# Kernel tuning notes

Measured on AMD Instinct MI355X. Metric: run time of the kernel, lower is better.

## Reference

```python
import jax, jax.numpy as jnp
import numpy as np

B, S, H, NH, HD = 2, 2048, 4096, 32, 128
THETA = 10000.0


def rotate_half(x):
    x1, x2 = jnp.split(x, 2, axis=-1)
    return jnp.concatenate((-x2, x1), axis=-1)


def setup_inputs() -> dict:
    key = jax.random.key(0)
    ks = jax.random.split(key, 6)
    hidden_states = jax.random.normal(ks[0], (B, S, H), dtype=jnp.float32)
    # additive causal mask, [1,1,S,S]
    causal = jnp.triu(jnp.full((S, S), -1e9, dtype=jnp.float32), k=1)
    attention_mask = causal[None, None, :, :]
    scale = 0.02
    Wq = jax.random.normal(ks[1], (H, H), dtype=jnp.float32) * scale
    Wk = jax.random.normal(ks[2], (H, H), dtype=jnp.float32) * scale
    Wv = jax.random.normal(ks[3], (H, H), dtype=jnp.float32) * scale
    Wo = jax.random.normal(ks[4], (H, H), dtype=jnp.float32) * scale
    return {"hidden_states": hidden_states, "attention_mask": attention_mask,
            "Wq": Wq, "Wk": Wk, "Wv": Wv, "Wo": Wo}


def _rope_tables(seq_len, dtype):
    inv_freq = 1.0 / (THETA ** (jnp.arange(0, HD, 2, dtype=jnp.float32) / HD))
    t = jnp.arange(seq_len, dtype=jnp.float32)
    freqs = jnp.einsum('i,j->ij', t, inv_freq)          # [S, HD/2]
    emb = jnp.concatenate((freqs, freqs), axis=-1)       # [S, HD]
    return jnp.cos(emb).astype(dtype), jnp.sin(emb).astype(dtype)


def reference(hidden_states, attention_mask, Wq, Wk, Wv, Wo):
    b, s, _ = hidden_states.shape
    # nn.Linear: y = x @ W.T
    q = jnp.einsum('bsh,oh->bso', hidden_states, Wq).reshape(b, s, NH, HD).transpose(0, 2, 1, 3)
    k = jnp.einsum('bsh,oh->bso', hidden_states, Wk).reshape(b, s, NH, HD).transpose(0, 2, 1, 3)
    v = jnp.einsum('bsh,oh->bso', hidden_states, Wv).reshape(b, s, NH, HD).transpose(0, 2, 1, 3)
    cos, sin = _rope_tables(s, q.dtype)                  # [S, HD] broadcast over b,h
    q = q * cos + rotate_half(q) * sin
    k = k * cos + rotate_half(k) * sin
    scores = jnp.einsum('bhqd,bhkd->bhqk', q, k) / jnp.sqrt(jnp.asarray(HD, q.dtype))
    scores = scores + attention_mask
    attn = jax.nn.softmax(scores.astype(jnp.float32), axis=-1).astype(q.dtype)
    out = jnp.einsum('bhqk,bhkd->bhqd', attn, v)
    out = out.transpose(0, 2, 1, 3).reshape(b, s, H)
    return jnp.einsum('bsh,oh->bso', out, Wo)
```

## Files before the change

kernel.cpp:

```cpp
#include <hip/hip_runtime.h>
#include <stdint.h>

typedef __attribute__((ext_vector_type(4))) float f32x4;
typedef __attribute__((ext_vector_type(8))) short bf16x8;
typedef __attribute__((ext_vector_type(4))) unsigned int u32x4;

__device__ __forceinline__ short f2bf(float x) {
  unsigned int u = __builtin_bit_cast(unsigned int, x);
  unsigned int r = (u + 0x7fffu + ((u >> 16) & 1u)) >> 16;
  return (short)r;
}
__device__ __forceinline__ float bf2f(short s) {
  unsigned int u = ((unsigned int)(unsigned short)s) << 16;
  return __builtin_bit_cast(float, u);
}
__device__ __forceinline__ unsigned pkbf(float lo, float hi) {
  unsigned r;
  asm("v_cvt_pk_bf16_f32 %0, %1, %2" : "=v"(r) : "v"(lo), "v"(hi));
  return r;
}

__device__ __forceinline__ void gload_lds16(const void* g, void* l) {
  __builtin_amdgcn_global_load_lds(
      (const __attribute__((address_space(1))) void*)g,
      (__attribute__((address_space(3))) void*)l, 16, 0, 0);
}

#define BARX() do { __builtin_amdgcn_s_barrier(); asm volatile("" ::: "memory"); } while (0)

__global__ __launch_bounds__(256) void cvt5(const float* __restrict__ a,
                                            const float* __restrict__ b,
                                            const float* __restrict__ c,
                                            const float* __restrict__ d,
                                            const float* __restrict__ e,
                                            short* __restrict__ oa,
                                            short* __restrict__ ob,
                                            short* __restrict__ oc,
                                            short* __restrict__ od,
                                            short* __restrict__ oe, int n) {
  int y = blockIdx.y;
  const float* in = (y == 0) ? a : (y == 1) ? b : (y == 2) ? c : (y == 3) ? d : e;
  short* out = (y == 0) ? oa : (y == 1) ? ob : (y == 2) ? oc : (y == 3) ? od : oe;
  int idx = blockIdx.x * blockDim.x + threadIdx.x;
  int stride = gridDim.x * blockDim.x;
  for (int i = idx * 4; i < n; i += stride * 4) {
    float4 v = *(const float4*)(in + i);
    short4 o;
    o.x = f2bf(v.x); o.y = f2bf(v.y); o.z = f2bf(v.z); o.w = f2bf(v.w);
    *(short4*)(out + i) = o;
  }
}

__global__ __launch_bounds__(256) void cvt_bf16(const float* __restrict__ in,
                                                short* __restrict__ out, int n) {
  int idx = blockIdx.x * blockDim.x + threadIdx.x;
  int stride = gridDim.x * blockDim.x;
  for (int i = idx * 4; i < n; i += stride * 4) {
    float4 v = *(const float4*)(in + i);
    short4 o;
    o.x = f2bf(v.x); o.y = f2bf(v.y); o.z = f2bf(v.z); o.w = f2bf(v.w);
    *(short4*)(out + i) = o;
  }
}

__global__ __launch_bounds__(256) void rope_table_k(float2* __restrict__ tab) {
  int idx = blockIdx.x * 256 + threadIdx.x;
  int s = idx >> 6, j = idx & 63;
  float invf = powf(10000.0f, -((float)j) / 64.0f);
  float a = (float)s * invf;
  tab[idx] = make_float2(cosf(a), sinf(a));
}

__global__ __launch_bounds__(256) void rope_apply_k(short* __restrict__ Qb,
                                                    short* __restrict__ Kb,
                                                    const float2* __restrict__ tab) {
  bool isK = (blockIdx.y != 0);
  short* base = isK ? Kb : Qb;
  float post = isK ? 1.0f : (0.08838834764831845f * 1.4426950408889634f);
  int token = blockIdx.x;
  int s = token & 2047;
  short* rowp = base + (size_t)token * 4096;
  const float2* trow = tab + s * 64;
  for (int u = threadIdx.x; u < 512; u += 256) {
    int h = u >> 4;
    int d0 = (u & 15) * 4;
    short* p1 = rowp + h * 128 + d0;
    short* p2 = p1 + 64;
    short4 a = *(short4*)p1, b = *(short4*)p2;
    short4 ra, rb;
#pragma unroll
    for (int j = 0; j < 4; ++j) {
      short aj = (&a.x)[j], bj = (&b.x)[j];
      float qa = bf2f(aj), qb = bf2f(bj);
      float2 cs = trow[d0 + j];
      (&ra.x)[j] = f2bf((qa * cs.x - qb * cs.y) * post);
      (&rb.x)[j] = f2bf((qb * cs.x + qa * cs.y) * post);
    }
    *(short4*)p1 = ra;
    *(short4*)p2 = rb;
  }
}

template <int MODE>
__global__ __launch_bounds__(512) void gemm8p(const short* __restrict__ A,
                                              const short* __restrict__ Bw,
                                              void* __restrict__ out) {
  __shared__ __attribute__((aligned(16))) short smem[2 * 32768];
  int wg = blockIdx.x;
  int xcd = wg & 7, ii = wg >> 3;
  int by = xcd * 2 + (ii >> 4);
  int bx = ii & 15;
  int tid = threadIdx.x;
  int w = tid >> 6, lane = tid & 63;
  int l16 = lane & 15, l4 = lane >> 4;
  int wm = w >> 2, wn = w & 3;

  f32x4 acc[8][4] = {};

  const short* Ab = A + (size_t)(by * 256) * 4096;
  const short* Bb = Bw + (size_t)(bx * 256) * 4096;

  auto STAGE_MAT = [&](int kt, int isB) {
    const short* src = isB ? Bb : Ab;
    int ob = (kt & 1) * 32768 + isB * 16384;
#pragma unroll
    for (int j = 0; j < 4; ++j) {
      int c = j * 512 + tid;
      int row = c >> 3;
      int sc = (c & 7) ^ (row & 7);
      gload_lds16(src + (size_t)row * 4096 + kt * 64 + sc * 8, &smem[ob + c * 8]);
    }
  };

  auto COMPUTE = [&](int ob) {
    bf16x8 af[4], bfr[4];
#pragma unroll
    for (int kk = 0; kk < 2; ++kk) {
#pragma unroll
      for (int nf = 0; nf < 4; ++nf) {
        int row = wn * 64 + nf * 16 + l16;
        int phys = (kk * 4 + l4) ^ (row & 7);
        bfr[nf] = *(const bf16x8*)&smem[ob + 16384 + row * 64 + phys * 8];
      }
#pragma unroll
      for (int mh = 0; mh < 2; ++mh) {
#pragma unroll
        for (int mf = 0; mf < 4; ++mf) {
          int row = wm * 128 + mh * 64 + mf * 16 + l16;
          int phys = (kk * 4 + l4) ^ (row & 7);
          af[mf] = *(const bf16x8*)&smem[ob + row * 64 + phys * 8];
        }
        __builtin_amdgcn_s_setprio(1);
#pragma unroll
        for (int mf = 0; mf < 4; ++mf)
#pragma unroll
          for (int nf = 0; nf < 4; ++nf)
            acc[mh * 4 + mf][nf] =
                __builtin_amdgcn_mfma_f32_16x16x32_bf16(af[mf], bfr[nf], acc[mh * 4 + mf][nf], 0, 0, 0);
        __builtin_amdgcn_s_setprio(0);
      }
    }
  };

  STAGE_MAT(0, 0);
  STAGE_MAT(0, 1);
  STAGE_MAT(1, 0);
  asm volatile("s_waitcnt vmcnt(4)" ::: "memory");
  BARX();

  for (int t = 0; t < 64; ++t) {
    int ob = (t & 1) * 32768;
    if (t + 1 < 64) STAGE_MAT(t + 1, 1);
    COMPUTE(ob);
    BARX();
    if (t + 2 < 64) {
      STAGE_MAT(t + 2, 0);
      asm volatile("s_waitcnt vmcnt(4)" ::: "memory");
    } else if (t + 1 < 64) {
      asm volatile("s_waitcnt vmcnt(0)" ::: "memory");
    }
    if (t + 1 < 64) BARX();
  }

  int orow0 = by * 256 + wm * 128;
  int ocol0 = bx * 256 + wn * 64;
#pragma unroll
  for (int mf = 0; mf < 8; ++mf)
#pragma unroll
    for (int nf = 0; nf < 4; ++nf)
#pragma unroll
      for (int k = 0; k < 4; ++k) {
        int r = orow0 + mf * 16 + l4 * 4 + k;
        int c = ocol0 + nf * 16 + l16;
        float v = acc[mf][nf][k];
        if constexpr (MODE == 0) {
          ((short*)out)[(size_t)r * 4096 + c] = f2bf(v);
        } else if constexpr (MODE == 1) {
          ((float*)out)[(size_t)r * 4096 + c] = v;
        } else {
          int bb = r >> 11, ss = r & 2047;
          int h = c >> 7, d = c & 127;
          ((short*)out)[(((size_t)((bb * 32 + h) * 128 + d)) << 11) + ss] = f2bf(v);
        }
      }
}

__global__ __launch_bounds__(512, 4) void attn_k(const short* __restrict__ Qb,
                                                 const short* __restrict__ Kb,
                                                 const short* __restrict__ Vt,
                                                 short* __restrict__ AO) {
  __shared__ __attribute__((aligned(16))) short smem[24576];
  int p = blockIdx.x;
  int bh = p & 63;
  int qt = 15 - (p >> 6);
  int b = bh >> 5, h = bh & 31;
  int tid = threadIdx.x, w = tid >> 6, lane = tid & 63;
  int l16 = lane & 15, l4 = lane >> 4;

  const int nt = 2 * qt + 2;
  const int qbase = qt * 128 + w * 16;

  bf16x8 qf[4];
  {
    const short* Qg = Qb + (size_t)(b * 2048 + qbase + l16) * 4096 + h * 128 + l4 * 8;
#pragma unroll
    for (int kk = 0; kk < 4; ++kk) qf[kk] = *(const bf16x8*)(Qg + kk * 32);
  }

  f32x4 oacc[8] = {};
  float mrun = -1e30f, lsum = 0.f;

  const short* Kbase = Kb + (size_t)(b * 2048) * 4096 + h * 128;
  const short* Vbase = Vt + (size_t)bh * 128 * 2048;

  auto STAGE_K = [&](int t, int sel) {
    short* lK = &smem[sel * 8192];
#pragma unroll
    for (int j = 0; j < 2; ++j) {
      int c = j * 512 + tid;
      int row = c >> 4;
      int src = (c & 15) ^ (row & 15);
      gload_lds16(Kbase + (size_t)(t * 64 + row) * 4096 + src * 8, &lK[c * 8]);
    }
  };
  auto STAGE_V = [&](int t) {
    short* lV = &smem[16384];
#pragma unroll
    for (int j = 0; j < 2; ++j) {
      int c = j * 512 + tid;
      int row = c >> 3;
      int src = (c & 7) ^ (row & 7);
      gload_lds16(Vbase + (size_t)row * 2048 + t * 64 + src * 8, &lV[c * 8]);
    }
  };

  STAGE_V(0);
  STAGE_K(0, 0);
  STAGE_K(1, 1);

  const int src0 = l16 | ((2 * (l4 & 1)) << 4);
  const int src1 = src0 | 16;
  const bool hiA = (l4 >> 1) != 0;

  for (int t = 0; t < nt; ++t) {
    if (t == nt - 1)
      asm volatile("s_waitcnt vmcnt(0)" ::: "memory");
    else
      asm volatile("s_waitcnt vmcnt(2)" ::: "memory");
    __builtin_amdgcn_s_barrier();
    asm volatile("" ::: "memory");

    bool skip = (t * 64 > qbase + 15);
    if (!skip) {
      const short* lK = &smem[(t & 1) * 8192];
      const short* lV = &smem[16384];

      f32x4 sacc[4] = {};
#pragma unroll
      for (int kk = 0; kk < 4; ++kk) {
#pragma unroll
        for (int n4 = 0; n4 < 4; ++n4) {
          int row = n4 * 16 + l16;
          int phys = (kk * 4 + l4) ^ (row & 15);
          bf16x8 kf = *(const bf16x8*)&lK[row * 128 + phys * 8];
          sacc[n4] = __builtin_amdgcn_mfma_f32_16x16x32_bf16(kf, qf[kk], sacc[n4], 0, 0, 0);
        }
      }

      if (t * 64 + 63 > qbase) {
        int q = qbase + l16;
#pragma unroll
        for (int n4 = 0; n4 < 4; ++n4)
#pragma unroll
          for (int i = 0; i < 4; ++i) {
            int kv = t * 64 + n4 * 16 + l4 * 4 + i;
            if (kv > q) sacc[n4][i] = -1e30f;
          }
      }

      {
        float v0 = fmaxf(fmaxf(sacc[0][0], sacc[0][1]), fmaxf(sacc[0][2], sacc[0][3]));
        float v1 = fmaxf(fmaxf(sacc[1][0], sacc[1][1]), fmaxf(sacc[1][2], sacc[1][3]));
        float v2 = fmaxf(fmaxf(sacc[2][0], sacc[2][1]), fmaxf(sacc[2][2], sacc[2][3]));
        float v3 = fmaxf(fmaxf(sacc[3][0], sacc[3][1]), fmaxf(sacc[3][2], sacc[3][3]));
        float vm = fmaxf(fmaxf(v0, v1), fmaxf(v2, v3));
        vm = fmaxf(vm, __shfl_xor(vm, 16));
        vm = fmaxf(vm, __shfl_xor(vm, 32));
        if (!__all(vm - mrun <= 8.0f)) {
          float mnew = fmaxf(mrun, vm);
          float fsc = __builtin_amdgcn_exp2f(mrun - mnew);
          mrun = mnew;
          lsum *= fsc;
#pragma unroll
          for (int dg = 0; dg < 8; ++dg) oacc[dg] *= fsc;
        }
        float psum = 0.f;
#pragma unroll
        for (int n4 = 0; n4 < 4; ++n4)
#pragma unroll
          for (int i = 0; i < 4; ++i) {
            float e = __builtin_amdgcn_exp2f(sacc[n4][i] - mrun);
            sacc[n4][i] = e;
            psum += e;
          }
        psum += __shfl_xor(psum, 16);
        psum += __shfl_xor(psum, 32);
        lsum += psum;
      }

#pragma unroll
      for (int c = 0; c < 2; ++c) {
        unsigned pk0h0 = pkbf(sacc[2 * c][0], sacc[2 * c][1]);
        unsigned pk0h1 = pkbf(sacc[2 * c][2], sacc[2 * c][3]);
        unsigned pk1h0 = pkbf(sacc[2 * c + 1][0], sacc[2 * c + 1][1]);
        unsigned pk1h1 = pkbf(sacc[2 * c + 1][2], sacc[2 * c + 1][3]);
        unsigned s00 = __shfl((int)pk0h0, src0), s10 = __shfl((int)pk1h0, src0);
        unsigned s01 = __shfl((int)pk0h1, src0), s11 = __shfl((int)pk1h1, src0);
        unsigned t00 = __shfl((int)pk0h0, src1), t10 = __shfl((int)pk1h0, src1);
        unsigned t01 = __shfl((int)pk0h1, src1), t11 = __shfl((int)pk1h1, src1);
        u32x4 uw;
        uw[0] = hiA ? s10 : s00;
        uw[1] = hiA ? s11 : s01;
        uw[2] = hiA ? t10 : t00;
        uw[3] = hiA ? t11 : t01;
        bf16x8 pb = __builtin_bit_cast(bf16x8, uw);
#pragma unroll
        for (int dg = 0; dg < 8; ++dg) {
          int d = dg * 16 + l16;
          int phys = (c * 4 + l4) ^ (l16 & 7);
          bf16x8 vf = *(const bf16x8*)&lV[d * 64 + phys * 8];
          oacc[dg] = __builtin_amdgcn_mfma_f32_16x16x32_bf16(vf, pb, oacc[dg], 0, 0, 0);
        }
      }
    }

    __builtin_amdgcn_s_barrier();
    asm volatile("" ::: "memory");
    if (t + 1 < nt) STAGE_V(t + 1);
    if (t + 2 < nt) STAGE_K(t + 2, t & 1);
  }

  __syncthreads();
  short* reg = &smem[w * 2048];
  float rls = 1.0f / lsum;
#pragma unroll
  for (int dg = 0; dg < 8; ++dg) {
    unsigned u0 = pkbf(oacc[dg][0] * rls, oacc[dg][1] * rls);
    unsigned u1 = pkbf(oacc[dg][2] * rls, oacc[dg][3] * rls);
    int cc = dg * 2 + (l4 >> 1);
    int phys = cc ^ l16;
    int sidx = l16 * 128 + phys * 8 + (l4 & 1) * 4;
    *(uint2*)&reg[sidx] = make_uint2(u0, u1);
  }
#pragma unroll
  for (int pass = 0; pass < 4; ++pass) {
    int qloc = pass * 4 + l4;
    int phys = l16 ^ qloc;
    bf16x8 v = *(const bf16x8*)&reg[qloc * 128 + phys * 8];
    int tok = b * 2048 + qbase + qloc;
    *(bf16x8*)(AO + (size_t)tok * 4096 + h * 128 + l16 * 8) = v;
  }
}

extern "C" void kernel_launch(void* const* d_in, const int* in_sizes, int n_in,
                              void* d_out, int out_size, void* d_ws, size_t ws_size,
                              hipStream_t stream) {
  const float* X = (const float*)d_in[0];
  const float* Wq = (const float*)d_in[2];
  const float* Wk = (const float*)d_in[3];
  const float* Wv = (const float*)d_in[4];
  const float* Wo = (const float*)d_in[5];

  char* ws = (char*)d_ws;
  const size_t SEG = 32ull << 20;
  short* Xb  = (short*)(ws + 0 * SEG);
  short* Wqb = (short*)(ws + 1 * SEG);
  short* Wkb = (short*)(ws + 2 * SEG);
  short* Wvb = (short*)(ws + 3 * SEG);
  short* Qb  = (short*)(ws + 4 * SEG);
  short* Kb  = (short*)(ws + 5 * SEG);
  float2* tab = (float2*)(ws + 6 * SEG);

  bool bigws = ws_size >= 6 * SEG + (4ull << 20) + SEG;
  short* WobBig = (short*)(ws + 6 * SEG + (4ull << 20));

  const int NE = 4096 * 4096;
  if (bigws) {
    cvt5<<<dim3(2048, 5), 256, 0, stream>>>(X, Wq, Wk, Wv, Wo, Xb, Wqb, Wkb, Wvb, WobBig, NE);
  } else {
    cvt5<<<dim3(2048, 4), 256, 0, stream>>>(X, Wq, Wk, Wv, nullptr, Xb, Wqb, Wkb, Wvb, nullptr, NE);
  }
  rope_table_k<<<512, 256, 0, stream>>>(tab);

  gemm8p<0><<<256, 512, 0, stream>>>(Xb, Wqb, Qb);
  gemm8p<0><<<256, 512, 0, stream>>>(Xb, Wkb, Kb);
  short* Vtb = Wqb;
  gemm8p<2><<<256, 512, 0, stream>>>(Xb, Wvb, Vtb);

  rope_apply_k<<<dim3(4096, 2), 256, 0, stream>>>(Qb, Kb, tab);

  short* AO = Xb;
  attn_k<<<1024, 512, 0, stream>>>(Qb, Kb, Vtb, AO);

  short* Wob;
  if (bigws) {
    Wob = WobBig;
  } else {
    Wob = Wkb;
    cvt_bf16<<<2048, 256, 0, stream>>>(Wo, Wob, NE);
  }
  gemm8p<1><<<256, 512, 0, stream>>>(AO, Wob, (float*)d_out);
}
```

Before: 680.6 us.

## Shrink GEMM tiles to 128x256 with K-step 32 for higher occupancy

Replaces the 256x256, K=64 tile GEMM with a 128x256 tile stepping K by 32. Shared memory drops from 128KB to 48KB, with a new XOR swizzle and launch bounds of 4 blocks. The grid doubles to 512 blocks so each CU can hold more waves, aiming for better latency hiding and wave balance across 256 CUs. The cost is lower arithmetic intensity per tile, twice as many barriers per K, and more global and LDS traffic per FLOP.

New measurement: 833.8 us. +22.5%, slower.

```diff
diff --git a/kernel.cpp b/kernel.cpp
--- a/kernel.cpp
+++ b/kernel.cpp
@@ -102,90 +102,87 @@
 }
 
 template <int MODE>
-__global__ __launch_bounds__(512) void gemm8p(const short* __restrict__ A,
-                                              const short* __restrict__ Bw,
-                                              void* __restrict__ out) {
-  __shared__ __attribute__((aligned(16))) short smem[2 * 32768];
+__global__ __launch_bounds__(512, 4) void gemm2b(const short* __restrict__ A,
+                                                 const short* __restrict__ Bw,
+                                                 void* __restrict__ out) {
+  __shared__ __attribute__((aligned(16))) short smem[2 * 12288];
   int wg = blockIdx.x;
   int xcd = wg & 7, ii = wg >> 3;
-  int by = xcd * 2 + (ii >> 4);
+  int by = xcd * 4 + (ii >> 4);
   int bx = ii & 15;
   int tid = threadIdx.x;
   int w = tid >> 6, lane = tid & 63;
   int l16 = lane & 15, l4 = lane >> 4;
   int wm = w >> 2, wn = w & 3;
 
-  f32x4 acc[8][4] = {};
-
-  const short* Ab = A + (size_t)(by * 256) * 4096;
+  f32x4 acc[4][4] = {};
+
+  const short* Ab = A + (size_t)(by * 128) * 4096;
   const short* Bb = Bw + (size_t)(bx * 256) * 4096;
 
-  auto STAGE_MAT = [&](int kt, int isB) {
-    const short* src = isB ? Bb : Ab;
-    int ob = (kt & 1) * 32768 + isB * 16384;
-#pragma unroll
-    for (int j = 0; j < 4; ++j) {
+  auto STAGE = [&](int t) {
+    int ob = (t & 1) * 12288;
+    {
+      int c = tid;
+      int row = c >> 2;
+      int gc = (c & 3) ^ ((row ^ (row >> 2)) & 3);
+      gload_lds16(Ab + (size_t)row * 4096 + t * 32 + gc * 8, &smem[ob + c * 8]);
+    }
+#pragma unroll
+    for (int j = 0; j < 2; ++j) {
       int c = j * 512 + tid;
-      int row = c >> 3;
-      int sc = (c & 7) ^ (row & 7);
-      gload_lds16(src + (size_t)row * 4096 + kt * 64 + sc * 8, &smem[ob + c * 8]);
+      int row = c >> 2;
+      int gc = (c & 3) ^ ((row ^ (row >> 2)) & 3);
+      gload_lds16(Bb + (size_t)row * 4096 + t * 32 + gc * 8, &smem[ob + 4096 + c * 8]);
     }
   };
 
   auto COMPUTE = [&](int ob) {
+    const short* lA = &smem[ob];
+    const short* lB = &smem[ob + 4096];
     bf16x8 af[4], bfr[4];
 #pragma unroll
-    for (int kk = 0; kk < 2; ++kk) {
-#pragma unroll
-      for (int nf = 0; nf < 4; ++nf) {
-        int row = wn * 64 + nf * 16 + l16;
-        int phys = (kk * 4 + l4) ^ (row & 7);
-        bfr[nf] = *(const bf16x8*)&smem[ob + 16384 + row * 64 + phys * 8];
-      }
-#pragma unroll
-      for (int mh = 0; mh < 2; ++mh) {
-#pragma unroll
-        for (int mf = 0; mf < 4; ++mf) {
-          int row = wm * 128 + mh * 64 + mf * 16 + l16;
-          int phys = (kk * 4 + l4) ^ (row & 7);
-          af[mf] = *(const bf16x8*)&smem[ob + row * 64 + phys * 8];
-        }
-        __builtin_amdgcn_s_setprio(1);
-#pragma unroll
-        for (int mf = 0; mf < 4; ++mf)
-#pragma unroll
-          for (int nf = 0; nf < 4; ++nf)
-            acc[mh * 4 + mf][nf] =
-                __builtin_amdgcn_mfma_f32_16x16x32_bf16(af[mf], bfr[nf], acc[mh * 4 + mf][nf], 0, 0, 0);
-        __builtin_amdgcn_s_setprio(0);
-      }
-    }
+    for (int nf = 0; nf < 4; ++nf) {
+      int row = wn * 64 + nf * 16 + l16;
+      int phys = l4 ^ ((row ^ (row >> 2)) & 3);
+      bfr[nf] = *(const bf16x8*)&lB[row * 32 + phys * 8];
+    }
+#pragma unroll
+    for (int mf = 0; mf < 4; ++mf) {
+      int row = wm * 64 + mf * 16 + l16;
+      int phys = l4 ^ ((row ^ (row >> 2)) & 3);
+      af[mf] = *(const bf16x8*)&lA[row * 32 + phys * 8];
+    }
+    __builtin_amdgcn_s_setprio(1);
+#pragma unroll
+    for (int mf = 0; mf < 4; ++mf)
+#pragma unroll
+      for (int nf = 0; nf < 4; ++nf)
+        acc[mf][nf] = __builtin_amdgcn_mfma_f32_16x16x32_bf16(af[mf], bfr[nf], acc[mf][nf], 0, 0, 0);
+    __builtin_amdgcn_s_setprio(0);
   };
 
-  STAGE_MAT(0, 0);
-  STAGE_MAT(0, 1);
-  STAGE_MAT(1, 0);
-  asm volatile("s_waitcnt vmcnt(4)" ::: "memory");
+  STAGE(0);
+  STAGE(1);
+  asm volatile("s_waitcnt vmcnt(3)" ::: "memory");
   BARX();
 
-  for (int t = 0; t < 64; ++t) {
-    int ob = (t & 1) * 32768;
-    if (t + 1 < 64) STAGE_MAT(t + 1, 1);
-    COMPUTE(ob);
+  for (int t = 0; t < 128; ++t) {
+    COMPUTE((t & 1) * 12288);
     BARX();
-    if (t + 2 < 64) {
-      STAGE_MAT(t + 2, 0);
-      asm volatile("s_waitcnt vmcnt(4)" ::: "memory");
-    } else if (t + 1 < 64) {
+    if (t + 2 < 128) {
+      STAGE(t + 2);
+      asm volatile("s_waitcnt vmcnt(3)" ::: "memory");
+    } else if (t + 1 < 128) {
       asm volatile("s_waitcnt vmcnt(0)" ::: "memory");
     }
-    if (t + 1 < 64) BARX();
-  }
-
-  int orow0 = by * 256 + wm * 128;
+    if (t + 1 < 128) BARX();
+  }
+
+  int orow0 = by * 128 + wm * 64;
   int ocol0 = bx * 256 + wn * 64;
 #pragma unroll
-  for (int mf = 0; mf < 8; ++mf)
+  for (int mf = 0; mf < 4; ++mf)
 #pragma unroll
     for (int nf = 0; nf < 4; ++nf)
 #pragma unroll
@@ -412,10 +409,10 @@
   }
   rope_table_k<<<512, 256, 0, stream>>>(tab);
 
-  gemm8p<0><<<256, 512, 0, stream>>>(Xb, Wqb, Qb);
-  gemm8p<0><<<256, 512, 0, stream>>>(Xb, Wkb, Kb);
+  gemm2b<0><<<512, 512, 0, stream>>>(Xb, Wqb, Qb);
+  gemm2b<0><<<512, 512, 0, stream>>>(Xb, Wkb, Kb);
   short* Vtb = Wqb;
-  gemm8p<2><<<256, 512, 0, stream>>>(Xb, Wvb, Vtb);
+  gemm2b<2><<<512, 512, 0, stream>>>(Xb, Wvb, Vtb);
 
   rope_apply_k<<<dim3(4096, 2), 256, 0, stream>>>(Qb, Kb, tab);
 
@@ -429,5 +426,5 @@
     Wob = Wkb;
     cvt_bf16<<<2048, 256, 0, stream>>>(Wo, Wob, NE);
   }
-  gemm8p<1><<<256, 512, 0, stream>>>(AO, Wob, (float*)d_out);
-}
+  gemm2b<1><<<512, 512, 0, stream>>>(AO, Wob, (float*)d_out);
+}
```
